# Kernel tuning notes

Measured on AMD Instinct MI355X. Metric: run time of the kernel, lower is better.

Reference implementation:

```python
import jax, jax.numpy as jnp
import numpy as np
import math

B, S, D, H, E = 4, 4096, 256, 8, 262144
HD = D // H
ITER_NUM = 4
TEMP = 1.0
LN_EPS = 1e-12
N = B * S


def setup_inputs() -> dict:
    key = jax.random.key(0)
    ks = jax.random.split(key, 6)
    return {
        "hidden_states": jax.random.normal(ks[0], (B, S, D), dtype=jnp.float32),
        "attention_mask": jnp.zeros((B, S), dtype=jnp.float32),
        "src": jax.random.randint(ks[1], (E,), 0, N),
        "dst": jax.random.randint(ks[2], (E,), 0, N),
        "Wqkv": jax.random.normal(ks[3], (D, 3 * D), dtype=jnp.float32) * 0.02,
        "bqkv": jnp.zeros((3 * D,), dtype=jnp.float32),
        "Wo": jax.random.normal(ks[4], (D, D), dtype=jnp.float32) * 0.02,
        "bo": jnp.zeros((D,), dtype=jnp.float32),
        "gamma": jnp.ones((D,), dtype=jnp.float32),
        "beta": jnp.zeros((D,), dtype=jnp.float32),
    }


def _gn_attn(hidden_states, attention_mask, src, dst, Wqkv, bqkv, Wo, bo, gamma, beta):
    # qkv projection (node ordering is batch-major: node = b*S + s)
    qkv = hidden_states @ Wqkv + bqkv                      # [B,S,3D]
    q, k, v = jnp.split(qkv, 3, axis=-1)
    q = q / math.sqrt(HD)
    qn = q.reshape(N, H, HD)
    kn = k.reshape(N, H, HD)
    vn = v.reshape(N, H, HD)
    node_mask = (attention_mask >= 0).reshape(N)           # [N] bool

    # per-edge dot-product scores: u_dot_v('k','q') -> dot(k[src], q[dst])
    score = jnp.einsum("ehd,ehd->eh", kn[src], qn[dst])    # [E,H]
    edge_mask = node_mask[src] & node_mask[dst]
    score = jnp.where(edge_mask[:, None], score, jnp.float32(-10000.0))

    # edge softmax over incoming edges of each dst node (per head)
    mx = jax.ops.segment_max(score, dst, num_segments=N)   # [N,H]
    es = jnp.exp(score - mx[dst])
    den = jax.ops.segment_sum(es, dst, num_segments=N)     # [N,H]
    attn = es / den[dst]                                   # [E,H]

    # diffusion (heat-kernel / PPR-style) message passing
    h = math.exp(-TEMP) * vn                               # [N,H,HD]
    gather = h
    fact = 1.0
    for ki in range(1, ITER_NUM):
        msg = attn[:, :, None] * h[src]                    # [E,H,HD]
        h = jax.ops.segment_sum(msg, dst, num_segments=N)  # [N,H,HD]
        fact = fact * (TEMP / ki)
        gather = gather + fact * h

    attn_out = gather.reshape(B, S, D)

    # output projection + residual + LayerNorm
    y = attn_out @ Wo + bo + hidden_states
    mu = jnp.mean(y, axis=-1, keepdims=True)
    var = jnp.mean(jnp.square(y - mu), axis=-1, keepdims=True)
    return (y - mu) / jnp.sqrt(var + LN_EPS) * gamma + beta


def reference(hidden_states, attention_mask, src, dst, Wqkv, bqkv, Wo, bo, gamma, beta):
    return _gn_attn(hidden_states, attention_mask, src, dst, Wqkv, bqkv, Wo, bo, gamma, beta)
```

## Files before the change

kernel.cpp:

```cpp
#include <hip/hip_runtime.h>
#include <math.h>

#define NN 16384
#define DD 256
#define HH 8
#define EE 262144
#define D3 768
#define MAXDEG 64
#define QSCALE 0.17677669529663687f
#define EXPN1 0.36787944117144233f
#define LN_EPS 1e-12f

typedef short bf16x8 __attribute__((ext_vector_type(8)));
typedef float f32x4 __attribute__((ext_vector_type(4)));
typedef float f32x2 __attribute__((ext_vector_type(2)));
typedef unsigned short u16;
typedef unsigned char u8;

__device__ __forceinline__ float bf_lo(unsigned u) { return __uint_as_float(u << 16); }
__device__ __forceinline__ float bf_hi(unsigned u) { return __uint_as_float(u & 0xffff0000u); }
__device__ __forceinline__ float bf16f(u16 u) { return __uint_as_float(((unsigned)u) << 16); }
__device__ __forceinline__ unsigned f2bf(float f) {
    unsigned b = __float_as_uint(f);
    return (b + 0x7fffu + ((b >> 16) & 1u)) >> 16;
}
__device__ __forceinline__ unsigned pack2bf(float lo, float hi) {
    return f2bf(lo) | (f2bf(hi) << 16);
}
__device__ __forceinline__ u8 f2fp8(float v) {
    return (u8)(__builtin_amdgcn_cvt_pk_fp8_f32(v, v, 0, false) & 0xff);
}
__device__ __forceinline__ void gload_lds16(const void* g, void* l) {
    __builtin_amdgcn_global_load_lds(
        (const __attribute__((address_space(1))) unsigned*)g,
        (__attribute__((address_space(3))) unsigned*)l, 16, 0, 0);
}

__global__ void prep_kernel(const float* __restrict__ hidden, unsigned* __restrict__ hidb,
                            const float* __restrict__ Wqkv, const float* __restrict__ bqkv,
                            u16* __restrict__ WtQ, float* __restrict__ biasq,
                            const float* __restrict__ Wo, const float* __restrict__ bo,
                            u16* __restrict__ WtO, float* __restrict__ biaso) {
    int b = blockIdx.x;
    if (b < 4096) {
        int gid = b * 256 + threadIdx.x;
        float4 v = *(const float4*)(hidden + (size_t)gid * 4);
        *(uint2*)(hidb + (size_t)gid * 2) = make_uint2(pack2bf(v.x, v.y), pack2bf(v.z, v.w));
    } else if (b < 4864) {
        int gid = (b - 4096) * 256 + threadIdx.x;
        int n = gid >> 8, k = gid & 255;
        float s = (n < DD) ? QSCALE : 1.0f;
        WtQ[(size_t)n * 256 + k] = (u16)f2bf(Wqkv[(size_t)k * D3 + n] * s);
        if (k == 0) biasq[n] = bqkv[n] * s;
    } else {
        int gid = (b - 4864) * 256 + threadIdx.x;
        int n = gid >> 8, k = gid & 255;
        WtO[(size_t)n * 256 + k] = (u16)f2bf(Wo[(size_t)k * DD + n]);
        if (k == 0) biaso[n] = bo[n];
    }
}

__global__ __launch_bounds__(256) void gemm1_scatter_kernel(
        const u16* __restrict__ Ab, const u16* __restrict__ Bt,
        const float* __restrict__ bias,
        u16* __restrict__ qb, u8* __restrict__ kb8,
        u8* __restrict__ h8, u16* __restrict__ gb,
        const int* __restrict__ src, const int* __restrict__ dst,
        int* __restrict__ cnt, int* __restrict__ srcs_pad) {
    __shared__ u16 As[128 * 32];
    __shared__ u16 Bs[128 * 32];
    if (blockIdx.x < 1024) {
        int e = blockIdx.x * 256 + threadIdx.x;
        int d = dst[e];
        int pos = atomicAdd(&cnt[d], 1);
        if (pos < MAXDEG) srcs_pad[d * MAXDEG + pos] = src[e];
        return;
    }
    const int bid = blockIdx.x - 1024;
    const int tid = threadIdx.x;
    const int m0 = (bid / 6) * 128;
    const int n0 = (bid % 6) * 128;
    const int wave = tid >> 6, lane = tid & 63;
    const int wr = wave >> 1, wc = wave & 1;
    const int lm = lane & 15, quad = lane >> 4;

    f32x4 acc[4][4] = {};
    const int srow = wave * 32 + (lane >> 2);
    const int scol = (lane & 3) * 8;

    for (int k0 = 0; k0 < 256; k0 += 32) {
        gload_lds16(Ab + (size_t)(m0 + srow) * 256 + k0 + scol,      &As[(wave * 32) * 32]);
        gload_lds16(Ab + (size_t)(m0 + srow + 16) * 256 + k0 + scol, &As[(wave * 32 + 16) * 32]);
        gload_lds16(Bt + (size_t)(n0 + srow) * 256 + k0 + scol,      &Bs[(wave * 32) * 32]);
        gload_lds16(Bt + (size_t)(n0 + srow + 16) * 256 + k0 + scol, &Bs[(wave * 32 + 16) * 32]);
        __syncthreads();
        bf16x8 af[4], bfv[4];
        #pragma unroll
        for (int mi = 0; mi < 4; ++mi)
            af[mi] = *(const bf16x8*)&As[(wr * 64 + mi * 16 + lm) * 32 + quad * 8];
        #pragma unroll
        for (int ni = 0; ni < 4; ++ni)
            bfv[ni] = *(const bf16x8*)&Bs[(wc * 64 + ni * 16 + lm) * 32 + quad * 8];
        #pragma unroll
        for (int mi = 0; mi < 4; ++mi)
            #pragma unroll
            for (int ni = 0; ni < 4; ++ni)
                acc[mi][ni] = __builtin_amdgcn_mfma_f32_16x16x32_bf16(
                    af[mi], bfv[ni], acc[mi][ni], 0, 0, 0);
        __syncthreads();
    }

    const int type = n0 >> 8;
    const int cb = n0 & 255;
    #pragma unroll
    for (int mi = 0; mi < 4; ++mi) {
        #pragma unroll
        for (int j = 0; j < 4; ++j) {
            int m = m0 + wr * 64 + mi * 16 + quad * 4 + j;
            #pragma unroll
            for (int ni = 0; ni < 4; ++ni) {
                int nl = wc * 64 + ni * 16 + lm;
                float val = acc[mi][ni][j] + bias[n0 + nl];
                size_t off = (size_t)m * 256 + cb + nl;
                if (type == 0) qb[off] = (u16)f2bf(val);
                else if (type == 1) kb8[off] = f2fp8(val);
                else {
                    float hx = val * EXPN1;
                    h8[off] = f2fp8(hx);
                    gb[off] = (u16)f2bf(hx);
                }
            }
        }
    }
}

__device__ __forceinline__ float edge_score(const unsigned qq[16], const u8* __restrict__ kb8,
                                            const float* __restrict__ amask,
                                            int s, int h, bool dvalid) {
    const uint4* kp = (const uint4*)(kb8 + (size_t)s * 256 + h * 32);
    uint4 k0 = kp[0], k1 = kp[1];
    unsigned kk[8] = {k0.x, k0.y, k0.z, k0.w, k1.x, k1.y, k1.z, k1.w};
    float acc = 0.0f;
    #pragma unroll
    for (int t = 0; t < 8; ++t) {
        f32x2 a = __builtin_amdgcn_cvt_pk_f32_fp8(kk[t], false);
        f32x2 b = __builtin_amdgcn_cvt_pk_f32_fp8(kk[t], true);
        acc += a.x * bf_lo(qq[2 * t]) + a.y * bf_hi(qq[2 * t]);
        acc += b.x * bf_lo(qq[2 * t + 1]) + b.y * bf_hi(qq[2 * t + 1]);
    }
    bool valid = dvalid && (amask[s] >= 0.0f);
    return valid ? acc : -10000.0f;
}

__global__ __launch_bounds__(256) void softmax_diffuse1_kernel(
        const unsigned* __restrict__ qb, const u8* __restrict__ kb8,
        const int* __restrict__ deg, const int* __restrict__ srcs_pad,
        const float* __restrict__ amask, u16* __restrict__ attn16,
        const unsigned* __restrict__ hA, unsigned* __restrict__ hB,
        uint2* __restrict__ gb) {
    __shared__ int   s_src[4][MAXDEG];
    __shared__ float s_att[4][MAXDEG * 8];
    const int wave = threadIdx.x >> 6, lane = threadIdx.x & 63;
    const int node = blockIdx.x * 4 + wave;
    const int h = lane & 7;
    const int eo = lane >> 3;
    const int beg = node * MAXDEG;
    int cnt = deg[node]; if (cnt > MAXDEG) cnt = MAXDEG;
    const int j2 = lane;
    uint2 g = gb[(size_t)node * 64 + j2];
    int sv = (lane < cnt) ? srcs_pad[beg + lane] : 0;
    s_src[wave][lane] = sv;

    const uint4* qp = (const uint4*)(qb + (size_t)node * 128 + h * 16);
    uint4 q0 = qp[0], q1 = qp[1], q2 = qp[2], q3 = qp[3];
    unsigned qq[16] = {q0.x, q0.y, q0.z, q0.w, q1.x, q1.y, q1.z, q1.w,
                       q2.x, q2.y, q2.z, q2.w, q3.x, q3.y, q3.z, q3.w};
    const bool dvalid = amask[node] >= 0.0f;

    float esb[8];
    float m = -1e30f;
    #pragma unroll
    for (int it = 0; it < 8; ++it) {
        int e = it * 8 + eo;
        int s = __shfl(sv, e);
        float sc = -1e30f;
        if (e < cnt) sc = edge_score(qq, kb8, amask, s, h, dvalid);
        esb[it] = sc;
        m = fmaxf(m, sc);
    }
    m = fmaxf(m, __shfl_xor(m, 8));
    m = fmaxf(m, __shfl_xor(m, 16));
    m = fmaxf(m, __shfl_xor(m, 32));
    float den = 0.0f;
    #pragma unroll
    for (int it = 0; it < 8; ++it) {
        int e = it * 8 + eo;
        if (e < cnt) { float es = __expf(esb[it] - m); esb[it] = es; den += es; }
    }
    den += __shfl_xor(den, 8);
    den += __shfl_xor(den, 16);
    den += __shfl_xor(den, 32);
    float iv = (cnt > 0) ? 1.0f / den : 0.0f;
    #pragma unroll
    for (int it = 0; it < 8; ++it) {
        int e = it * 8 + eo;
        float a = (e < cnt) ? esb[it] * iv : 0.0f;
        attn16[(size_t)(beg + e) * 8 + h] = (u16)f2bf(a);
        s_att[wave][e * 8 + h] = a;
    }
    __syncthreads();

    const int hh = j2 >> 3;
    float a0 = 0.0f, a1 = 0.0f, a2 = 0.0f, a3 = 0.0f;
    for (int e0 = 0; e0 < cnt; e0 += 8) {
        int sa[8]; float aa[8]; unsigned hv[8];
        #pragma unroll
        for (int t = 0; t < 8; ++t) {
            sa[t] = s_src[wave][e0 + t];
            aa[t] = s_att[wave][(e0 + t) * 8 + hh];
        }
        #pragma unroll
        for (int t = 0; t < 8; ++t)
            hv[t] = hA[(size_t)sa[t] * 64 + j2];
        #pragma unroll
        for (int t = 0; t < 8; ++t) {
            float a = aa[t];
            f32x2 lo = __builtin_amdgcn_cvt_pk_f32_fp8(hv[t], false);
            f32x2 hi = __builtin_amdgcn_cvt_pk_f32_fp8(hv[t], true);
            a0 += a * lo.x; a1 += a * lo.y;
            a2 += a * hi.x; a3 += a * hi.y;
        }
    }
    int pk = __builtin_amdgcn_cvt_pk_fp8_f32(a0, a1, 0, false);
    pk = __builtin_amdgcn_cvt_pk_fp8_f32(a2, a3, pk, true);
    hB[(size_t)node * 64 + j2] = (unsigned)pk;
    float g0 = bf_lo(g.x) + a0;
    float g1 = bf_hi(g.x) + a1;
    float g2 = bf_lo(g.y) + a2;
    float g3 = bf_hi(g.y) + a3;
    gb[(size_t)node * 64 + j2] = make_uint2(pack2bf(g0, g1), pack2bf(g2, g3));
}

__global__ void diffuse2_kernel(const int* __restrict__ deg, const int* __restrict__ srcs_pad,
                                const u16* __restrict__ attn16,
                                const unsigned* __restrict__ hcur,
                                unsigned* __restrict__ hnext) {
    int gid = blockIdx.x * 256 + threadIdx.x;
    int node = gid >> 6;
    int j2 = gid & 63;
    int h = j2 >> 3;
    int beg = node * MAXDEG;
    int cnt = deg[node]; if (cnt > MAXDEG) cnt = MAXDEG;
    int sv = (j2 < cnt) ? srcs_pad[beg + j2] : 0;
    const u16* ap = attn16 + (size_t)beg * 8;
    float a0 = 0.0f, a1 = 0.0f, a2 = 0.0f, a3 = 0.0f;
    for (int e0 = 0; e0 < cnt; e0 += 8) {
        float aval = bf16f(ap[e0 * 8 + j2]);
        unsigned hv[8]; float aa[8];
        #pragma unroll
        for (int t = 0; t < 8; ++t) {
            int s = __shfl(sv, e0 + t);
            aa[t] = __shfl(aval, t * 8 + h);
            hv[t] = hcur[(size_t)s * 64 + j2];
        }
        #pragma unroll
        for (int t = 0; t < 8; ++t) {
            float a = aa[t];
            f32x2 lo = __builtin_amdgcn_cvt_pk_f32_fp8(hv[t], false);
            f32x2 hi = __builtin_amdgcn_cvt_pk_f32_fp8(hv[t], true);
            a0 += a * lo.x; a1 += a * lo.y;
            a2 += a * hi.x; a3 += a * hi.y;
        }
    }
    int pk = __builtin_amdgcn_cvt_pk_fp8_f32(a0, a1, 0, false);
    pk = __builtin_amdgcn_cvt_pk_fp8_f32(a2, a3, pk, true);
    hnext[(size_t)node * 64 + j2] = (unsigned)pk;
}

__global__ void diffuse3_kernel(const int* __restrict__ deg, const int* __restrict__ srcs_pad,
                                const u16* __restrict__ attn16,
                                const unsigned* __restrict__ h2buf,
                                uint2* __restrict__ gb) {
    int gid = blockIdx.x * 256 + threadIdx.x;
    int node = gid >> 6;
    int j2 = gid & 63;
    int h = j2 >> 3;
    int beg = node * MAXDEG;
    int cnt = deg[node]; if (cnt > MAXDEG) cnt = MAXDEG;
    uint2* gp = gb + (size_t)node * 64 + j2;
    uint2 g = *gp;
    unsigned h2own = h2buf[(size_t)node * 64 + j2];
    int sv = (j2 < cnt) ? srcs_pad[beg + j2] : 0;
    const u16* ap = attn16 + (size_t)beg * 8;
    float a0 = 0.0f, a1 = 0.0f, a2 = 0.0f, a3 = 0.0f;
    for (int e0 = 0; e0 < cnt; e0 += 8) {
        float aval = bf16f(ap[e0 * 8 + j2]);
        unsigned hv[8]; float aa[8];
        #pragma unroll
        for (int t = 0; t < 8; ++t) {
            int s = __shfl(sv, e0 + t);
            aa[t] = __shfl(aval, t * 8 + h);
            hv[t] = h2buf[(size_t)s * 64 + j2];
        }
        #pragma unroll
        for (int t = 0; t < 8; ++t) {
            float a = aa[t];
            f32x2 lo = __builtin_amdgcn_cvt_pk_f32_fp8(hv[t], false);
            f32x2 hi = __builtin_amdgcn_cvt_pk_f32_fp8(hv[t], true);
            a0 += a * lo.x; a1 += a * lo.y;
            a2 += a * hi.x; a3 += a * hi.y;
        }
    }
    f32x2 h2lo = __builtin_amdgcn_cvt_pk_f32_fp8(h2own, false);
    f32x2 h2hi = __builtin_amdgcn_cvt_pk_f32_fp8(h2own, true);
    const float f3 = 1.0f / 6.0f;
    float g0 = bf_lo(g.x) + 0.5f * h2lo.x + f3 * a0;
    float g1 = bf_hi(g.x) + 0.5f * h2lo.y + f3 * a1;
    float g2 = bf_lo(g.y) + 0.5f * h2hi.x + f3 * a2;
    float g3 = bf_hi(g.y) + 0.5f * h2hi.y + f3 * a3;
    *gp = make_uint2(pack2bf(g0, g1), pack2bf(g2, g3));
}

__global__ __launch_bounds__(256) void gemm2_ln_kernel(
        const u16* __restrict__ Ab, const u16* __restrict__ Bt,
        const float* __restrict__ bias, const float* __restrict__ resid,
        const float* __restrict__ gamma, const float* __restrict__ beta,
        float* __restrict__ out) {
    __shared__ u16 As[64 * 32];
    __shared__ u16 Bs[256 * 32];
    const int tid = threadIdx.x;
    const int m0 = blockIdx.x * 64;
    const int wave = tid >> 6, lane = tid & 63;
    const int lm = lane & 15, quad = lane >> 4;
    const int lrow = lane >> 2;
    const int scol = (lane & 3) * 8;

    f32x4 acc[16] = {};
    for (int k0 = 0; k0 < 256; k0 += 32) {
        gload_lds16(Ab + (size_t)(m0 + wave * 16 + lrow) * 256 + k0 + scol,
                    &As[(wave * 16) * 32]);
        #pragma unroll
        for (int i = 0; i < 4; ++i)
            gload_lds16(Bt + (size_t)(wave * 64 + i * 16 + lrow) * 256 + k0 + scol,
                        &Bs[(wave * 64 + i * 16) * 32]);
        __syncthreads();
        bf16x8 af = *(const bf16x8*)&As[(wave * 16 + lm) * 32 + quad * 8];
        #pragma unroll
        for (int ni = 0; ni < 16; ++ni) {
            bf16x8 bfv = *(const bf16x8*)&Bs[(ni * 16 + lm) * 32 + quad * 8];
            acc[ni] = __builtin_amdgcn_mfma_f32_16x16x32_bf16(af, bfv, acc[ni], 0, 0, 0);
        }
        __syncthreads();
    }

    const int mrow = m0 + wave * 16 + quad * 4;
    float ga[16], be[16];
    float rowsum[4] = {}, rowsq[4] = {};
    #pragma unroll
    for (int ni = 0; ni < 16; ++ni) {
        int col = ni * 16 + lm;
        float bia = bias[col];
        ga[ni] = gamma[col]; be[ni] = beta[col];
        #pragma unroll
        for (int j = 0; j < 4; ++j) {
            float val = acc[ni][j] + bia + resid[(size_t)(mrow + j) * 256 + col];
            acc[ni][j] = val;
            rowsum[j] += val;
            rowsq[j] += val * val;
        }
    }
    #pragma unroll
    for (int j = 0; j < 4; ++j) {
        #pragma unroll
        for (int msk = 1; msk <= 8; msk <<= 1) {
            rowsum[j] += __shfl_xor(rowsum[j], msk);
            rowsq[j] += __shfl_xor(rowsq[j], msk);
        }
    }
    float mu[4], rstd[4];
    #pragma unroll
    for (int j = 0; j < 4; ++j) {
        mu[j] = rowsum[j] * (1.0f / 256.0f);
        float var = rowsq[j] * (1.0f / 256.0f) - mu[j] * mu[j];
        rstd[j] = 1.0f / sqrtf(var + LN_EPS);
    }
    #pragma unroll
    for (int ni = 0; ni < 16; ++ni) {
        int col = ni * 16 + lm;
        #pragma unroll
        for (int j = 0; j < 4; ++j)
            out[(size_t)(mrow + j) * 256 + col] = (acc[ni][j] - mu[j]) * rstd[j] * ga[ni] + be[ni];
    }
}

extern "C" void kernel_launch(void* const* d_in, const int* in_sizes, int n_in,
                              void* d_out, int out_size, void* d_ws, size_t ws_size,
                              hipStream_t stream) {
    const float* hidden = (const float*)d_in[0];
    const float* amask  = (const float*)d_in[1];
    const int*   src    = (const int*)d_in[2];
    const int*   dst    = (const int*)d_in[3];
    const float* Wqkv   = (const float*)d_in[4];
    const float* bqkv   = (const float*)d_in[5];
    const float* Wo     = (const float*)d_in[6];
    const float* bo     = (const float*)d_in[7];
    const float* gamma  = (const float*)d_in[8];
    const float* beta   = (const float*)d_in[9];
    float* out = (float*)d_out;

    char* p = (char*)d_ws;
    u16*      hidb   = (u16*)p;      p += (size_t)NN * DD * 2;
    u16*      WtQ    = (u16*)p;      p += (size_t)D3 * DD * 2;
    u16*      WtO    = (u16*)p;      p += (size_t)DD * DD * 2;
    float*    biasq  = (float*)p;    p += (size_t)D3 * 4;
    float*    biaso  = (float*)p;    p += (size_t)DD * 4;
    u16*      qb     = (u16*)p;      p += (size_t)NN * DD * 2;
    u8*       kb8    = (u8*)p;       p += (size_t)NN * DD;
    u8*       h8A    = (u8*)p;       p += (size_t)NN * DD;
    u8*       h8B    = (u8*)p;       p += (size_t)NN * DD;
    u8*       h8C    = (u8*)p;       p += (size_t)NN * DD;
    u16*      gb     = (u16*)p;      p += (size_t)NN * DD * 2;
    u16*      attn16 = (u16*)p;      p += (size_t)NN * MAXDEG * HH * 2;
    int*      cnt    = (int*)p;      p += (size_t)NN * 4;
    int*      srcs   = (int*)p;      p += (size_t)NN * MAXDEG * 4;

    hipMemsetAsync(cnt, 0, (size_t)NN * 4, stream);
    prep_kernel<<<5120, 256, 0, stream>>>(hidden, (unsigned*)hidb,
                                          Wqkv, bqkv, WtQ, biasq,
                                          Wo, bo, WtO, biaso);

    gemm1_scatter_kernel<<<1792, 256, 0, stream>>>(
        hidb, WtQ, biasq, qb, kb8, h8A, gb, src, dst, cnt, srcs);

    softmax_diffuse1_kernel<<<NN / 4, 256, 0, stream>>>(
        (const unsigned*)qb, kb8, cnt, srcs, amask, attn16,
        (const unsigned*)h8A, (unsigned*)h8B, (uint2*)gb);

    diffuse2_kernel<<<(NN * 64) / 256, 256, 0, stream>>>(
        cnt, srcs, attn16, (const unsigned*)h8B, (unsigned*)h8C);

    diffuse3_kernel<<<(NN * 64) / 256, 256, 0, stream>>>(
        cnt, srcs, attn16, (const unsigned*)h8C, (uint2*)gb);

    gemm2_ln_kernel<<<NN / 64, 256, 0, stream>>>(
        gb, WtO, biaso, hidden, gamma, beta, out);
}
```

Measured before the change: 181.1 us.

## Process two nodes per wave in diffusion kernels and fold cnt memset into prep

The diffusion-2 and diffusion-3 kernels now have each wave handle two destination nodes, w and w+8192, interleaving their gathers. The goal is more independent memory loads in flight per wave to hide gather latency, with half as many blocks launched. The count-buffer memset is replaced by extra blocks in the prep kernel, removing one separate launch. In exchange, each wave loops to the larger of the two node degrees, and register pressure goes up.

```diff
diff --git a/kernel.cpp b/kernel.cpp
--- a/kernel.cpp
+++ b/kernel.cpp
@@ -40,7 +40,8 @@
                             const float* __restrict__ Wqkv, const float* __restrict__ bqkv,
                             u16* __restrict__ WtQ, float* __restrict__ biasq,
                             const float* __restrict__ Wo, const float* __restrict__ bo,
-                            u16* __restrict__ WtO, float* __restrict__ biaso) {
+                            u16* __restrict__ WtO, float* __restrict__ biaso,
+                            int* __restrict__ cnt) {
     int b = blockIdx.x;
     if (b < 4096) {
         int gid = b * 256 + threadIdx.x;
@@ -52,11 +53,13 @@
         float s = (n < DD) ? QSCALE : 1.0f;
         WtQ[(size_t)n * 256 + k] = (u16)f2bf(Wqkv[(size_t)k * D3 + n] * s);
         if (k == 0) biasq[n] = bqkv[n] * s;
-    } else {
+    } else if (b < 5120) {
         int gid = (b - 4864) * 256 + threadIdx.x;
         int n = gid >> 8, k = gid & 255;
         WtO[(size_t)n * 256 + k] = (u16)f2bf(Wo[(size_t)k * DD + n]);
         if (k == 0) biaso[n] = bo[n];
+    } else {
+        cnt[(b - 5120) * 256 + threadIdx.x] = 0;
     }
 }
 
@@ -245,80 +248,120 @@
                                 const u16* __restrict__ attn16,
                                 const unsigned* __restrict__ hcur,
                                 unsigned* __restrict__ hnext) {
-    int gid = blockIdx.x * 256 + threadIdx.x;
-    int node = gid >> 6;
-    int j2 = gid & 63;
+    int w = blockIdx.x * 4 + (threadIdx.x >> 6);
+    int j2 = threadIdx.x & 63;
     int h = j2 >> 3;
-    int beg = node * MAXDEG;
-    int cnt = deg[node]; if (cnt > MAXDEG) cnt = MAXDEG;
-    int sv = (j2 < cnt) ? srcs_pad[beg + j2] : 0;
-    const u16* ap = attn16 + (size_t)beg * 8;
-    float a0 = 0.0f, a1 = 0.0f, a2 = 0.0f, a3 = 0.0f;
-    for (int e0 = 0; e0 < cnt; e0 += 8) {
-        float aval = bf16f(ap[e0 * 8 + j2]);
-        unsigned hv[8]; float aa[8];
-        #pragma unroll
-        for (int t = 0; t < 8; ++t) {
-            int s = __shfl(sv, e0 + t);
-            aa[t] = __shfl(aval, t * 8 + h);
-            hv[t] = hcur[(size_t)s * 64 + j2];
-        }
-        #pragma unroll
-        for (int t = 0; t < 8; ++t) {
-            float a = aa[t];
-            f32x2 lo = __builtin_amdgcn_cvt_pk_f32_fp8(hv[t], false);
-            f32x2 hi = __builtin_amdgcn_cvt_pk_f32_fp8(hv[t], true);
-            a0 += a * lo.x; a1 += a * lo.y;
-            a2 += a * hi.x; a3 += a * hi.y;
-        }
-    }
-    int pk = __builtin_amdgcn_cvt_pk_fp8_f32(a0, a1, 0, false);
-    pk = __builtin_amdgcn_cvt_pk_fp8_f32(a2, a3, pk, true);
-    hnext[(size_t)node * 64 + j2] = (unsigned)pk;
+    int nA = w, nB = w + 8192;
+    int begA = nA * MAXDEG, begB = nB * MAXDEG;
+    int cA = deg[nA]; if (cA > MAXDEG) cA = MAXDEG;
+    int cB = deg[nB]; if (cB > MAXDEG) cB = MAXDEG;
+    int svA = (j2 < cA) ? srcs_pad[begA + j2] : 0;
+    int svB = (j2 < cB) ? srcs_pad[begB + j2] : 0;
+    const u16* apA = attn16 + (size_t)begA * 8;
+    const u16* apB = attn16 + (size_t)begB * 8;
+    float a0A = 0, a1A = 0, a2A = 0, a3A = 0;
+    float a0B = 0, a1B = 0, a2B = 0, a3B = 0;
+    int nc = cA > cB ? cA : cB;
+    for (int e0 = 0; e0 < nc; e0 += 8) {
+        float avA = bf16f(apA[e0 * 8 + j2]);
+        float avB = bf16f(apB[e0 * 8 + j2]);
+        unsigned hvA[8], hvB[8]; float aaA[8], aaB[8];
+        #pragma unroll
+        for (int t = 0; t < 8; ++t) {
+            int sA = __shfl(svA, e0 + t);
+            int sB = __shfl(svB, e0 + t);
+            hvA[t] = hcur[(size_t)sA * 64 + j2];
+            hvB[t] = hcur[(size_t)sB * 64 + j2];
+            aaA[t] = __shfl(avA, t * 8 + h);
+            aaB[t] = __shfl(avB, t * 8 + h);
+        }
+        #pragma unroll
+        for (int t = 0; t < 8; ++t) {
+            f32x2 loA = __builtin_amdgcn_cvt_pk_f32_fp8(hvA[t], false);
+            f32x2 hiA = __builtin_amdgcn_cvt_pk_f32_fp8(hvA[t], true);
+            a0A += aaA[t] * loA.x; a1A += aaA[t] * loA.y;
+            a2A += aaA[t] * hiA.x; a3A += aaA[t] * hiA.y;
+            f32x2 loB = __builtin_amdgcn_cvt_pk_f32_fp8(hvB[t], false);
+            f32x2 hiB = __builtin_amdgcn_cvt_pk_f32_fp8(hvB[t], true);
+            a0B += aaB[t] * loB.x; a1B += aaB[t] * loB.y;
+            a2B += aaB[t] * hiB.x; a3B += aaB[t] * hiB.y;
+        }
+    }
+    int pkA = __builtin_amdgcn_cvt_pk_fp8_f32(a0A, a1A, 0, false);
+    pkA = __builtin_amdgcn_cvt_pk_fp8_f32(a2A, a3A, pkA, true);
+    hnext[(size_t)nA * 64 + j2] = (unsigned)pkA;
+    int pkB = __builtin_amdgcn_cvt_pk_fp8_f32(a0B, a1B, 0, false);
+    pkB = __builtin_amdgcn_cvt_pk_fp8_f32(a2B, a3B, pkB, true);
+    hnext[(size_t)nB * 64 + j2] = (unsigned)pkB;
 }
 
 __global__ void diffuse3_kernel(const int* __restrict__ deg, const int* __restrict__ srcs_pad,
                                 const u16* __restrict__ attn16,
                                 const unsigned* __restrict__ h2buf,
                                 uint2* __restrict__ gb) {
-    int gid = blockIdx.x * 256 + threadIdx.x;
-    int node = gid >> 6;
-    int j2 = gid & 63;
+    int w = blockIdx.x * 4 + (threadIdx.x >> 6);
+    int j2 = threadIdx.x & 63;
     int h = j2 >> 3;
-    int beg = node * MAXDEG;
-    int cnt = deg[node]; if (cnt > MAXDEG) cnt = MAXDEG;
-    uint2* gp = gb + (size_t)node * 64 + j2;
-    uint2 g = *gp;
-    unsigned h2own = h2buf[(size_t)node * 64 + j2];
-    int sv = (j2 < cnt) ? srcs_pad[beg + j2] : 0;
-    const u16* ap = attn16 + (size_t)beg * 8;
-    float a0 = 0.0f, a1 = 0.0f, a2 = 0.0f, a3 = 0.0f;
-    for (int e0 = 0; e0 < cnt; e0 += 8) {
-        float aval = bf16f(ap[e0 * 8 + j2]);
-        unsigned hv[8]; float aa[8];
-        #pragma unroll
-        for (int t = 0; t < 8; ++t) {
-            int s = __shfl(sv, e0 + t);
-            aa[t] = __shfl(aval, t * 8 + h);
-            hv[t] = h2buf[(size_t)s * 64 + j2];
-        }
-        #pragma unroll
-        for (int t = 0; t < 8; ++t) {
-            float a = aa[t];
-            f32x2 lo = __builtin_amdgcn_cvt_pk_f32_fp8(hv[t], false);
-            f32x2 hi = __builtin_amdgcn_cvt_pk_f32_fp8(hv[t], true);
-            a0 += a * lo.x; a1 += a * lo.y;
-            a2 += a * hi.x; a3 += a * hi.y;
-        }
-    }
-    f32x2 h2lo = __builtin_amdgcn_cvt_pk_f32_fp8(h2own, false);
-    f32x2 h2hi = __builtin_amdgcn_cvt_pk_f32_fp8(h2own, true);
+    int nA = w, nB = w + 8192;
+    int begA = nA * MAXDEG, begB = nB * MAXDEG;
+    int cA = deg[nA]; if (cA > MAXDEG) cA = MAXDEG;
+    int cB = deg[nB]; if (cB > MAXDEG) cB = MAXDEG;
+    uint2* gpA = gb + (size_t)nA * 64 + j2;
+    uint2* gpB = gb + (size_t)nB * 64 + j2;
+    uint2 gA = *gpA, gB = *gpB;
+    unsigned h2ownA = h2buf[(size_t)nA * 64 + j2];
+    unsigned h2ownB = h2buf[(size_t)nB * 64 + j2];
+    int svA = (j2 < cA) ? srcs_pad[begA + j2] : 0;
+    int svB = (j2 < cB) ? srcs_pad[begB + j2] : 0;
+    const u16* apA = attn16 + (size_t)begA * 8;
+    const u16* apB = attn16 + (size_t)begB * 8;
+    float a0A = 0, a1A = 0, a2A = 0, a3A = 0;
+    float a0B = 0, a1B = 0, a2B = 0, a3B = 0;
+    int nc = cA > cB ? cA : cB;
+    for (int e0 = 0; e0 < nc; e0 += 8) {
+        float avA = bf16f(apA[e0 * 8 + j2]);
+        float avB = bf16f(apB[e0 * 8 + j2]);
+        unsigned hvA[8], hvB[8]; float aaA[8], aaB[8];
+        #pragma unroll
+        for (int t = 0; t < 8; ++t) {
+            int sA = __shfl(svA, e0 + t);
+            int sB = __shfl(svB, e0 + t);
+            hvA[t] = h2buf[(size_t)sA * 64 + j2];
+            hvB[t] = h2buf[(size_t)sB * 64 + j2];
+            aaA[t] = __shfl(avA, t * 8 + h);
+            aaB[t] = __shfl(avB, t * 8 + h);
+        }
+        #pragma unroll
+        for (int t = 0; t < 8; ++t) {
+            f32x2 loA = __builtin_amdgcn_cvt_pk_f32_fp8(hvA[t], false);
+            f32x2 hiA = __builtin_amdgcn_cvt_pk_f32_fp8(hvA[t], true);
+            a0A += aaA[t] * loA.x; a1A += aaA[t] * loA.y;
+            a2A += aaA[t] * hiA.x; a3A += aaA[t] * hiA.y;
+            f32x2 loB = __builtin_amdgcn_cvt_pk_f32_fp8(hvB[t], false);
+            f32x2 hiB = __builtin_amdgcn_cvt_pk_f32_fp8(hvB[t], true);
+            a0B += aaB[t] * loB.x; a1B += aaB[t] * loB.y;
+            a2B += aaB[t] * hiB.x; a3B += aaB[t] * hiB.y;
+        }
+    }
     const float f3 = 1.0f / 6.0f;
-    float g0 = bf_lo(g.x) + 0.5f * h2lo.x + f3 * a0;
-    float g1 = bf_hi(g.x) + 0.5f * h2lo.y + f3 * a1;
-    float g2 = bf_lo(g.y) + 0.5f * h2hi.x + f3 * a2;
-    float g3 = bf_hi(g.y) + 0.5f * h2hi.y + f3 * a3;
-    *gp = make_uint2(pack2bf(g0, g1), pack2bf(g2, g3));
+    {
+        f32x2 h2lo = __builtin_amdgcn_cvt_pk_f32_fp8(h2ownA, false);
+        f32x2 h2hi = __builtin_amdgcn_cvt_pk_f32_fp8(h2ownA, true);
+        float g0 = bf_lo(gA.x) + 0.5f * h2lo.x + f3 * a0A;
+        float g1 = bf_hi(gA.x) + 0.5f * h2lo.y + f3 * a1A;
+        float g2 = bf_lo(gA.y) + 0.5f * h2hi.x + f3 * a2A;
+        float g3 = bf_hi(gA.y) + 0.5f * h2hi.y + f3 * a3A;
+        *gpA = make_uint2(pack2bf(g0, g1), pack2bf(g2, g3));
+    }
+    {
+        f32x2 h2lo = __builtin_amdgcn_cvt_pk_f32_fp8(h2ownB, false);
+        f32x2 h2hi = __builtin_amdgcn_cvt_pk_f32_fp8(h2ownB, true);
+        float g0 = bf_lo(gB.x) + 0.5f * h2lo.x + f3 * a0B;
+        float g1 = bf_hi(gB.x) + 0.5f * h2lo.y + f3 * a1B;
+        float g2 = bf_lo(gB.y) + 0.5f * h2hi.x + f3 * a2B;
+        float g3 = bf_hi(gB.y) + 0.5f * h2hi.y + f3 * a3B;
+        *gpB = make_uint2(pack2bf(g0, g1), pack2bf(g2, g3));
+    }
 }
 
 __global__ __launch_bounds__(256) void gemm2_ln_kernel(
@@ -424,10 +467,9 @@
     int*      cnt    = (int*)p;      p += (size_t)NN * 4;
     int*      srcs   = (int*)p;      p += (size_t)NN * MAXDEG * 4;
 
-    hipMemsetAsync(cnt, 0, (size_t)NN * 4, stream);
-    prep_kernel<<<5120, 256, 0, stream>>>(hidden, (unsigned*)hidb,
+    prep_kernel<<<5184, 256, 0, stream>>>(hidden, (unsigned*)hidb,
                                           Wqkv, bqkv, WtQ, biasq,
-                                          Wo, bo, WtO, biaso);
+                                          Wo, bo, WtO, biaso, cnt);
 
     gemm1_scatter_kernel<<<1792, 256, 0, stream>>>(
         hidb, WtQ, biasq, qb, kb8, h8A, gb, src, dst, cnt, srcs);
@@ -436,10 +478,10 @@
         (const unsigned*)qb, kb8, cnt, srcs, amask, attn16,
         (const unsigned*)h8A, (unsigned*)h8B, (uint2*)gb);
 
-    diffuse2_kernel<<<(NN * 64) / 256, 256, 0, stream>>>(
+    diffuse2_kernel<<<2048, 256, 0, stream>>>(
         cnt, srcs, attn16, (const unsigned*)h8B, (unsigned*)h8C);
 
-    diffuse3_kernel<<<(NN * 64) / 256, 256, 0, stream>>>(
+    diffuse3_kernel<<<2048, 256, 0, stream>>>(
         cnt, srcs, attn16, (const unsigned*)h8C, (uint2*)gb);
 
     gemm2_ln_kernel<<<NN / 64, 256, 0, stream>>>(
```

Result: no change. 183.3 us (+1.2%).
